# Optimization experiments

Measured on AMD Instinct MI355X. Metric: run time of the kernel, lower is better.

## Reference

```python
import jax, jax.numpy as jnp
import numpy as np

T, TOPK = 512, 2
E, H, D = 8, 2816, 1024


def setup_inputs() -> dict:
    key = jax.random.key(0)
    k1, k2, k3, k4, k5 = jax.random.split(key, 5)
    x = jax.random.normal(k1, (T, D), dtype=jnp.float32)
    expert_indices = jax.random.randint(k2, (T, TOPK), 0, E, dtype=jnp.int64)
    w1 = jax.random.normal(k3, (E, H, D), dtype=jnp.float32)
    w2 = jax.random.normal(k4, (E, H, D), dtype=jnp.float32)
    w3 = jax.random.normal(k5, (E, H, D), dtype=jnp.float32)
    return {"x": x, "expert_indices": expert_indices, "w1": w1, "w2": w2, "w3": w3}


def reference(x, expert_indices, w1, w2, w3):
    # Math identical to: silu(x @ w1[e].T) * (x @ w3[e].T) @ w2[e] for e = expert_indices[t, a].
    # Computed densely over all experts (GEMM-friendly), then gathered per token,
    # which avoids materializing [T, a, H, D] gathered weight tensors.
    h1 = jax.nn.silu(jnp.einsum('ti,ehi->teh', x, w1))   # [T, E, H]
    h3 = jnp.einsum('ti,ehi->teh', x, w3)                # [T, E, H]
    out_all = jnp.einsum('teh,ehi->tei', h1 * h3, w2)    # [T, E, D]
    # gather the top_k selected experts per token -> [T, TOPK, D]
    idx = expert_indices[:, :, None]                     # [T, a, 1]
    expert_outs = jnp.take_along_axis(out_all, idx, axis=1)
    return expert_outs
```

## Files before the change

kernel.cpp:

```cpp
#include <hip/hip_runtime.h>


#define NEXP 8
#define HDIM 2816
#define DDIM 1024
#define NPAIR 1024

typedef unsigned int uint;
typedef unsigned short ushort;
typedef __attribute__((ext_vector_type(8))) short bf16x8;
typedef __attribute__((ext_vector_type(4))) float fvec4;
typedef __attribute__((ext_vector_type(4))) uint uvec4;

__device__ __forceinline__ ushort f2bf(float f) {
    uint u = __builtin_bit_cast(uint, f);
    u += 0x7fff + ((u >> 16) & 1);
    return (ushort)(u >> 16);
}
__device__ __forceinline__ uint pack2(float lo, float hi) {
    return (uint)f2bf(lo) | ((uint)f2bf(hi) << 16);
}
__device__ __forceinline__ uvec4 pack8(fvec4 a, fvec4 b) {
    uvec4 v;
    v.x = pack2(a.x, a.y); v.y = pack2(a.z, a.w);
    v.z = pack2(b.x, b.y); v.w = pack2(b.z, b.w);
    return v;
}

__device__ __forceinline__ void wg_sync_lds() {
    __builtin_amdgcn_sched_barrier(0);
    asm volatile("s_waitcnt lgkmcnt(0)" ::: "memory");
    __builtin_amdgcn_s_barrier();
    __builtin_amdgcn_sched_barrier(0);
}

__global__ __launch_bounds__(1024) void route_kernel(const int* __restrict__ idx,
                                                     int* __restrict__ counts,
                                                     int* __restrict__ lists) {
    int p = threadIdx.x;
    if (p < NEXP) counts[p] = 0;
    __syncthreads();
    int e = idx[p];
    int pos = atomicAdd(&counts[e], 1);
    lists[e * NPAIR + pos] = p;
}

#define LDK 68

#define NCH1 (DDIM / 64)

__global__ __launch_bounds__(512, 4) void h_mfma(const float* __restrict__ x,
                       const float* __restrict__ w1,
                       const float* __restrict__ w3,
                       const int* __restrict__ counts,
                       const int* __restrict__ lists,
                       ushort* __restrict__ hb) {
    const int e = blockIdx.x;
    const int cnt = counts[e];
    const int m0 = blockIdx.z * 128;
    if (m0 >= cnt) return;
    const int h0 = blockIdx.y * 32;

    __shared__ ushort sA[2][128 * LDK];
    __shared__ ushort sB[2][2][32 * LDK];
    __shared__ int sTok[128];
    __shared__ int sPairS[128];

    const int tid = threadIdx.x;
    if (tid < 128) {
        int m = m0 + tid;
        int mc = (m < cnt) ? m : (cnt - 1);
        int p = lists[e * NPAIR + mc];
        sTok[tid] = p >> 1;
        sPairS[tid] = (m < cnt) ? p : -1;
    }
    wg_sync_lds();

    const int arow = tid >> 2;
    const int akg  = (tid & 3) * 16;
    const float* aSrc = x + (size_t)sTok[arow] * DDIM + akg;

    const int bmat = tid >> 8;
    const int brow = (tid >> 3) & 31;
    const int bkg  = (tid & 7) * 8;
    const float* bSrc = (bmat ? w3 : w1) + (size_t)e * HDIM * DDIM
                        + (size_t)(h0 + brow) * DDIM + bkg;

    fvec4 pfA[2][4];
    fvec4 pfB[2][2];

#define P1_ISSUE(S, KC) do { \
    const float* qa = aSrc + (KC) * 64; \
    pfA[S][0] = *(const fvec4*)qa; \
    pfA[S][1] = *(const fvec4*)(qa + 4); \
    pfA[S][2] = *(const fvec4*)(qa + 8); \
    pfA[S][3] = *(const fvec4*)(qa + 12); \
    const float* qb = bSrc + (KC) * 64; \
    pfB[S][0] = *(const fvec4*)qb; \
    pfB[S][1] = *(const fvec4*)(qb + 4); \
} while (0)

#define P1_STAGE(S, B) do { \
    *(uvec4*)&sA[B][arow * LDK + akg] = pack8(pfA[S][0], pfA[S][1]); \
    *(uvec4*)&sA[B][arow * LDK + akg + 8] = pack8(pfA[S][2], pfA[S][3]); \
    *(uvec4*)&sB[B][bmat][brow * LDK + bkg] = pack8(pfB[S][0], pfB[S][1]); \
} while (0)

    const int w = tid >> 6;
    const int wm = w & 3;
    const int wh = w >> 2;
    const int lane = tid & 63;
    const int l16 = lane & 15;
    const int quad = lane >> 4;

    const int ar0 = (wm * 32 + l16) * LDK + quad * 8;
    const int br0 = (wh * 16 + l16) * LDK + quad * 8;

    fvec4 acc[2][2];
    #pragma unroll
    for (int i = 0; i < 2; ++i) { acc[i][0] = (fvec4)0.f; acc[i][1] = (fvec4)0.f; }

    P1_ISSUE(0, 0);
    P1_ISSUE(1, 1);
    P1_STAGE(0, 0);
    wg_sync_lds();

#define P1_BODY(T, CUR) do { \
    bf16x8 a00 = *(const bf16x8*)&sA[CUR][ar0]; \
    bf16x8 a01 = *(const bf16x8*)&sA[CUR][ar0 + 32]; \
    bf16x8 a10 = *(const bf16x8*)&sA[CUR][ar0 + 16 * LDK]; \
    bf16x8 a11 = *(const bf16x8*)&sA[CUR][ar0 + 16 * LDK + 32]; \
    bf16x8 b00 = *(const bf16x8*)&sB[CUR][0][br0]; \
    bf16x8 b01 = *(const bf16x8*)&sB[CUR][0][br0 + 32]; \
    bf16x8 b10 = *(const bf16x8*)&sB[CUR][1][br0]; \
    bf16x8 b11 = *(const bf16x8*)&sB[CUR][1][br0 + 32]; \
    if ((T) + 2 < NCH1) P1_ISSUE(CUR, (T) + 2); \
    acc[0][0] = __builtin_amdgcn_mfma_f32_16x16x32_bf16(a00, b00, acc[0][0], 0, 0, 0); \
    acc[0][1] = __builtin_amdgcn_mfma_f32_16x16x32_bf16(a00, b10, acc[0][1], 0, 0, 0); \
    acc[1][0] = __builtin_amdgcn_mfma_f32_16x16x32_bf16(a10, b00, acc[1][0], 0, 0, 0); \
    acc[1][1] = __builtin_amdgcn_mfma_f32_16x16x32_bf16(a10, b10, acc[1][1], 0, 0, 0); \
    acc[0][0] = __builtin_amdgcn_mfma_f32_16x16x32_bf16(a01, b01, acc[0][0], 0, 0, 0); \
    acc[0][1] = __builtin_amdgcn_mfma_f32_16x16x32_bf16(a01, b11, acc[0][1], 0, 0, 0); \
    acc[1][0] = __builtin_amdgcn_mfma_f32_16x16x32_bf16(a11, b01, acc[1][0], 0, 0, 0); \
    acc[1][1] = __builtin_amdgcn_mfma_f32_16x16x32_bf16(a11, b11, acc[1][1], 0, 0, 0); \
    if ((T) + 1 < NCH1) { \
        P1_STAGE(CUR ^ 1, CUR ^ 1); \
        wg_sync_lds(); \
    } \
} while (0)

    for (int t = 0; t < NCH1; t += 2) {
        P1_BODY(t, 0);
        P1_BODY(t + 1, 1);
    }

    #pragma unroll
    for (int mi = 0; mi < 2; ++mi) {
        #pragma unroll
        for (int r = 0; r < 4; ++r) {
            int mrow = wm * 32 + mi * 16 + quad * 4 + r;
            int p = sPairS[mrow];
            if (p >= 0) {
                float a = acc[mi][0][r];
                float g = acc[mi][1][r];
                float s = a / (1.f + __expf(-a)) * g;
                hb[(size_t)p * HDIM + h0 + wh * 16 + l16] = f2bf(s);
            }
        }
    }
}

#define NCH2 ((HDIM / 4) / 64)

__global__ __launch_bounds__(512, 4) void out_mfma(const float* __restrict__ w2,
                         const int* __restrict__ counts,
                         const int* __restrict__ lists,
                         const ushort* __restrict__ hb,
                         float* __restrict__ out) {
    const int e = blockIdx.x;
    const int cnt = counts[e];
    const int mb = blockIdx.z >> 2;
    const int sk = blockIdx.z & 3;
    const int m0 = mb * 128;
    if (m0 >= cnt) return;
    const int n0 = blockIdx.y * 32;
    const int kbase = sk * (HDIM / 4);

    __shared__ ushort sA[2][128 * LDK];
    __shared__ ushort sB[2][32 * LDK];
    __shared__ int sPairC[128];
    __shared__ int sPairS[128];

    const int tid = threadIdx.x;
    if (tid < 128) {
        int m = m0 + tid;
        int mc = (m < cnt) ? m : (cnt - 1);
        int p = lists[e * NPAIR + mc];
        sPairC[tid] = p;
        sPairS[tid] = (m < cnt) ? p : -1;
    }
    wg_sync_lds();

    const int arow = tid >> 2;
    const int akg  = (tid & 3) * 16;
    const ushort* aSrc = hb + (size_t)sPairC[arow] * HDIM + kbase + akg;

    const int bkp = (tid >> 3) & 31;
    const int bdg = tid & 7;
    const float* bSrc = w2 + (size_t)e * HDIM * DDIM
                        + (size_t)(kbase + 2 * bkp) * DDIM + n0 + bdg * 4;

    uvec4 pfA[2][2];
    fvec4 pfB[2][2];

#define P2_ISSUE(S, KC) do { \
    const ushort* qa = aSrc + (KC) * 64; \
    pfA[S][0] = *(const uvec4*)qa; \
    pfA[S][1] = *(const uvec4*)(qa + 8); \
    if (tid < 256) { \
        const float* qb = bSrc + (size_t)(KC) * 64 * DDIM; \
        pfB[S][0] = *(const fvec4*)qb; \
        pfB[S][1] = *(const fvec4*)(qb + DDIM); \
    } \
} while (0)

#define P2_STAGE(S, B) do { \
    *(uvec4*)&sA[B][arow * LDK + akg] = pfA[S][0]; \
    *(uvec4*)&sA[B][arow * LDK + akg + 8] = pfA[S][1]; \
    if (tid < 256) { \
        _Pragma("unroll") \
        for (int j = 0; j < 4; ++j) \
            *(uint*)&sB[B][(bdg * 4 + j) * LDK + bkp * 2] = pack2(pfB[S][0][j], pfB[S][1][j]); \
    } \
} while (0)

    const int w = tid >> 6;
    const int wm = w & 3;
    const int wh = w >> 2;
    const int lane = tid & 63;
    const int l16 = lane & 15;
    const int quad = lane >> 4;

    const int ar0 = (wm * 32 + l16) * LDK + quad * 8;
    const int br0 = (wh * 16 + l16) * LDK + quad * 8;

    fvec4 acc[2];
    acc[0] = (fvec4)0.f; acc[1] = (fvec4)0.f;

    P2_ISSUE(0, 0);
    P2_ISSUE(1, 1);
    P2_STAGE(0, 0);
    wg_sync_lds();

#define P2_BODY(T, CUR) do { \
    bf16x8 a00 = *(const bf16x8*)&sA[CUR][ar0]; \
    bf16x8 a01 = *(const bf16x8*)&sA[CUR][ar0 + 32]; \
    bf16x8 a10 = *(const bf16x8*)&sA[CUR][ar0 + 16 * LDK]; \
    bf16x8 a11 = *(const bf16x8*)&sA[CUR][ar0 + 16 * LDK + 32]; \
    bf16x8 b0 = *(const bf16x8*)&sB[CUR][br0]; \
    bf16x8 b1 = *(const bf16x8*)&sB[CUR][br0 + 32]; \
    if ((T) + 2 < NCH2) P2_ISSUE(CUR, (T) + 2); \
    acc[0] = __builtin_amdgcn_mfma_f32_16x16x32_bf16(a00, b0, acc[0], 0, 0, 0); \
    acc[1] = __builtin_amdgcn_mfma_f32_16x16x32_bf16(a10, b0, acc[1], 0, 0, 0); \
    acc[0] = __builtin_amdgcn_mfma_f32_16x16x32_bf16(a01, b1, acc[0], 0, 0, 0); \
    acc[1] = __builtin_amdgcn_mfma_f32_16x16x32_bf16(a11, b1, acc[1], 0, 0, 0); \
    if ((T) + 1 < NCH2) { \
        P2_STAGE(CUR ^ 1, CUR ^ 1); \
        wg_sync_lds(); \
    } \
} while (0)

    for (int t = 0; t < NCH2; t += 2) {
        P2_BODY(t, 0);
        if (t + 1 < NCH2) P2_BODY(t + 1, 1);
    }

    #pragma unroll
    for (int mi = 0; mi < 2; ++mi) {
        #pragma unroll
        for (int r = 0; r < 4; ++r) {
            int mrow = wm * 32 + mi * 16 + quad * 4 + r;
            int p = sPairS[mrow];
            if (p >= 0)
                atomicAdd(&out[(size_t)p * DDIM + n0 + wh * 16 + l16], acc[mi][r]);
        }
    }
}

extern "C" void kernel_launch(void* const* d_in, const int* in_sizes, int n_in,
                              void* d_out, int out_size, void* d_ws, size_t ws_size,
                              hipStream_t stream) {
    const float* x   = (const float*)d_in[0];
    const int*   idx = (const int*)d_in[1];
    const float* w1  = (const float*)d_in[2];
    const float* w2  = (const float*)d_in[3];
    const float* w3  = (const float*)d_in[4];
    float* out = (float*)d_out;

    char* ws = (char*)d_ws;
    int*    counts = (int*)ws;
    int*    lists  = (int*)(ws + 1024);
    ushort* hbuf   = (ushort*)(ws + 65536);

    hipMemsetAsync(out, 0, (size_t)out_size * sizeof(float), stream);
    route_kernel<<<1, NPAIR, 0, stream>>>(idx, counts, lists);
    h_mfma<<<dim3(NEXP, HDIM / 32, NPAIR / 128), 512, 0, stream>>>(
        x, w1, w3, counts, lists, hbuf);
    out_mfma<<<dim3(NEXP, DDIM / 32, (NPAIR / 128) * 4), 512, 0, stream>>>(
        w2, counts, lists, hbuf, out);
}
```

Baseline: 345.2 us.

## Load MFMA operands directly from global memory, dropping shared-LDS staging and barriers

Both GEMM kernels stop staging A and B tiles through shared LDS with workgroup barriers. Instead, each wave loads its MFMA fragments straight from global memory into registers, converting them to bf16 in registers. The output kernel uses a small per-wave swizzled LDS buffer to transpose w2. Blocks shrink to 256 threads with a 64-row M tile, and the output kernel's K split goes from 4 to 2. This removes barrier stalls and LDS traffic, but loses data reuse across waves, so the same x and weight rows are fetched by multiple waves through the cache.

```diff
diff --git a/kernel.cpp b/kernel.cpp
--- a/kernel.cpp
+++ b/kernel.cpp
@@ -20,18 +20,11 @@
 __device__ __forceinline__ uint pack2(float lo, float hi) {
     return (uint)f2bf(lo) | ((uint)f2bf(hi) << 16);
 }
-__device__ __forceinline__ uvec4 pack8(fvec4 a, fvec4 b) {
+__device__ __forceinline__ bf16x8 cvt8(fvec4 a, fvec4 b) {
     uvec4 v;
     v.x = pack2(a.x, a.y); v.y = pack2(a.z, a.w);
     v.z = pack2(b.x, b.y); v.w = pack2(b.z, b.w);
-    return v;
-}
-
-__device__ __forceinline__ void wg_sync_lds() {
-    __builtin_amdgcn_sched_barrier(0);
-    asm volatile("s_waitcnt lgkmcnt(0)" ::: "memory");
-    __builtin_amdgcn_s_barrier();
-    __builtin_amdgcn_sched_barrier(0);
+    return __builtin_bit_cast(bf16x8, v);
 }
 
 __global__ __launch_bounds__(1024) void route_kernel(const int* __restrict__ idx,
@@ -45,11 +38,9 @@
     lists[e * NPAIR + pos] = p;
 }
 
-#define LDK 68
-
-#define NCH1 (DDIM / 64)
-
-__global__ __launch_bounds__(512, 4) void h_mfma(const float* __restrict__ x,
+#define NCH1 32
+
+__global__ __launch_bounds__(256, 4) void h_mfma(const float* __restrict__ x,
                        const float* __restrict__ w1,
                        const float* __restrict__ w3,
                        const int* __restrict__ counts,
@@ -57,232 +48,165 @@
                        ushort* __restrict__ hb) {
     const int e = blockIdx.x;
     const int cnt = counts[e];
-    const int m0 = blockIdx.z * 128;
+    const int m0 = blockIdx.z * 64;
     if (m0 >= cnt) return;
     const int h0 = blockIdx.y * 32;
 
-    __shared__ ushort sA[2][128 * LDK];
-    __shared__ ushort sB[2][2][32 * LDK];
-    __shared__ int sTok[128];
-    __shared__ int sPairS[128];
-
     const int tid = threadIdx.x;
-    if (tid < 128) {
-        int m = m0 + tid;
-        int mc = (m < cnt) ? m : (cnt - 1);
-        int p = lists[e * NPAIR + mc];
-        sTok[tid] = p >> 1;
-        sPairS[tid] = (m < cnt) ? p : -1;
-    }
-    wg_sync_lds();
-
-    const int arow = tid >> 2;
-    const int akg  = (tid & 3) * 16;
-    const float* aSrc = x + (size_t)sTok[arow] * DDIM + akg;
-
-    const int bmat = tid >> 8;
-    const int brow = (tid >> 3) & 31;
-    const int bkg  = (tid & 7) * 8;
-    const float* bSrc = (bmat ? w3 : w1) + (size_t)e * HDIM * DDIM
-                        + (size_t)(h0 + brow) * DDIM + bkg;
-
-    fvec4 pfA[2][4];
-    fvec4 pfB[2][2];
-
-#define P1_ISSUE(S, KC) do { \
-    const float* qa = aSrc + (KC) * 64; \
-    pfA[S][0] = *(const fvec4*)qa; \
-    pfA[S][1] = *(const fvec4*)(qa + 4); \
-    pfA[S][2] = *(const fvec4*)(qa + 8); \
-    pfA[S][3] = *(const fvec4*)(qa + 12); \
-    const float* qb = bSrc + (KC) * 64; \
-    pfB[S][0] = *(const fvec4*)qb; \
-    pfB[S][1] = *(const fvec4*)(qb + 4); \
-} while (0)
-
-#define P1_STAGE(S, B) do { \
-    *(uvec4*)&sA[B][arow * LDK + akg] = pack8(pfA[S][0], pfA[S][1]); \
-    *(uvec4*)&sA[B][arow * LDK + akg + 8] = pack8(pfA[S][2], pfA[S][3]); \
-    *(uvec4*)&sB[B][bmat][brow * LDK + bkg] = pack8(pfB[S][0], pfB[S][1]); \
-} while (0)
-
-    const int w = tid >> 6;
-    const int wm = w & 3;
-    const int wh = w >> 2;
+    const int wm = (tid >> 6) & 1;
+    const int wh = tid >> 7;
     const int lane = tid & 63;
     const int l16 = lane & 15;
     const int quad = lane >> 4;
-
-    const int ar0 = (wm * 32 + l16) * LDK + quad * 8;
-    const int br0 = (wh * 16 + l16) * LDK + quad * 8;
+    const int mw = m0 + wm * 32;
+    const int hw = h0 + wh * 16;
+
+    const int* lst = lists + e * NPAIR;
+    int r0 = mw + l16;       int rc0 = (r0 < cnt) ? r0 : (cnt - 1);
+    int r1 = mw + 16 + l16;  int rc1 = (r1 < cnt) ? r1 : (cnt - 1);
+    const float* xa0 = x + (size_t)(lst[rc0] >> 1) * DDIM + quad * 8;
+    const float* xa1 = x + (size_t)(lst[rc1] >> 1) * DDIM + quad * 8;
+    const float* bp1 = w1 + (size_t)e * HDIM * DDIM + (size_t)(hw + l16) * DDIM + quad * 8;
+    const float* bp3 = w3 + (size_t)e * HDIM * DDIM + (size_t)(hw + l16) * DDIM + quad * 8;
+
+    fvec4 pf[2][8];
+
+#define H_ISSUE(S, K) do { \
+    pf[S][0] = *(const fvec4*)(xa0 + (K));     pf[S][1] = *(const fvec4*)(xa0 + (K) + 4); \
+    pf[S][2] = *(const fvec4*)(xa1 + (K));     pf[S][3] = *(const fvec4*)(xa1 + (K) + 4); \
+    pf[S][4] = *(const fvec4*)(bp1 + (K));     pf[S][5] = *(const fvec4*)(bp1 + (K) + 4); \
+    pf[S][6] = *(const fvec4*)(bp3 + (K));     pf[S][7] = *(const fvec4*)(bp3 + (K) + 4); \
+} while (0)
 
     fvec4 acc[2][2];
     #pragma unroll
     for (int i = 0; i < 2; ++i) { acc[i][0] = (fvec4)0.f; acc[i][1] = (fvec4)0.f; }
 
-    P1_ISSUE(0, 0);
-    P1_ISSUE(1, 1);
-    P1_STAGE(0, 0);
-    wg_sync_lds();
-
-#define P1_BODY(T, CUR) do { \
-    bf16x8 a00 = *(const bf16x8*)&sA[CUR][ar0]; \
-    bf16x8 a01 = *(const bf16x8*)&sA[CUR][ar0 + 32]; \
-    bf16x8 a10 = *(const bf16x8*)&sA[CUR][ar0 + 16 * LDK]; \
-    bf16x8 a11 = *(const bf16x8*)&sA[CUR][ar0 + 16 * LDK + 32]; \
-    bf16x8 b00 = *(const bf16x8*)&sB[CUR][0][br0]; \
-    bf16x8 b01 = *(const bf16x8*)&sB[CUR][0][br0 + 32]; \
-    bf16x8 b10 = *(const bf16x8*)&sB[CUR][1][br0]; \
-    bf16x8 b11 = *(const bf16x8*)&sB[CUR][1][br0 + 32]; \
-    if ((T) + 2 < NCH1) P1_ISSUE(CUR, (T) + 2); \
-    acc[0][0] = __builtin_amdgcn_mfma_f32_16x16x32_bf16(a00, b00, acc[0][0], 0, 0, 0); \
-    acc[0][1] = __builtin_amdgcn_mfma_f32_16x16x32_bf16(a00, b10, acc[0][1], 0, 0, 0); \
-    acc[1][0] = __builtin_amdgcn_mfma_f32_16x16x32_bf16(a10, b00, acc[1][0], 0, 0, 0); \
-    acc[1][1] = __builtin_amdgcn_mfma_f32_16x16x32_bf16(a10, b10, acc[1][1], 0, 0, 0); \
-    acc[0][0] = __builtin_amdgcn_mfma_f32_16x16x32_bf16(a01, b01, acc[0][0], 0, 0, 0); \
-    acc[0][1] = __builtin_amdgcn_mfma_f32_16x16x32_bf16(a01, b11, acc[0][1], 0, 0, 0); \
-    acc[1][0] = __builtin_amdgcn_mfma_f32_16x16x32_bf16(a11, b01, acc[1][0], 0, 0, 0); \
-    acc[1][1] = __builtin_amdgcn_mfma_f32_16x16x32_bf16(a11, b11, acc[1][1], 0, 0, 0); \
-    if ((T) + 1 < NCH1) { \
-        P1_STAGE(CUR ^ 1, CUR ^ 1); \
-        wg_sync_lds(); \
-    } \
+    H_ISSUE(0, 0);
+    H_ISSUE(1, 32);
+
+#define H_BODY(T, S) do { \
+    bf16x8 a0 = cvt8(pf[S][0], pf[S][1]); \
+    bf16x8 a1 = cvt8(pf[S][2], pf[S][3]); \
+    bf16x8 b1 = cvt8(pf[S][4], pf[S][5]); \
+    bf16x8 b3 = cvt8(pf[S][6], pf[S][7]); \
+    if ((T) + 2 < NCH1) H_ISSUE(S, ((T) + 2) * 32); \
+    acc[0][0] = __builtin_amdgcn_mfma_f32_16x16x32_bf16(a0, b1, acc[0][0], 0, 0, 0); \
+    acc[0][1] = __builtin_amdgcn_mfma_f32_16x16x32_bf16(a0, b3, acc[0][1], 0, 0, 0); \
+    acc[1][0] = __builtin_amdgcn_mfma_f32_16x16x32_bf16(a1, b1, acc[1][0], 0, 0, 0); \
+    acc[1][1] = __builtin_amdgcn_mfma_f32_16x16x32_bf16(a1, b3, acc[1][1], 0, 0, 0); \
 } while (0)
 
     for (int t = 0; t < NCH1; t += 2) {
-        P1_BODY(t, 0);
-        P1_BODY(t + 1, 1);
+        H_BODY(t, 0);
+        H_BODY(t + 1, 1);
     }
 
     #pragma unroll
     for (int mi = 0; mi < 2; ++mi) {
         #pragma unroll
         for (int r = 0; r < 4; ++r) {
-            int mrow = wm * 32 + mi * 16 + quad * 4 + r;
-            int p = sPairS[mrow];
-            if (p >= 0) {
+            int row = mw + mi * 16 + quad * 4 + r;
+            if (row < cnt) {
+                int p = lst[row];
                 float a = acc[mi][0][r];
                 float g = acc[mi][1][r];
                 float s = a / (1.f + __expf(-a)) * g;
-                hb[(size_t)p * HDIM + h0 + wh * 16 + l16] = f2bf(s);
+                hb[(size_t)p * HDIM + hw + l16] = f2bf(s);
             }
         }
     }
 }
 
-#define NCH2 ((HDIM / 4) / 64)
-
-__global__ __launch_bounds__(512, 4) void out_mfma(const float* __restrict__ w2,
+#define NCH2 ((HDIM / 2) / 64)
+
+__global__ __launch_bounds__(256, 4) void out_mfma(const float* __restrict__ w2,
                          const int* __restrict__ counts,
                          const int* __restrict__ lists,
                          const ushort* __restrict__ hb,
                          float* __restrict__ out) {
     const int e = blockIdx.x;
     const int cnt = counts[e];
-    const int mb = blockIdx.z >> 2;
-    const int sk = blockIdx.z & 3;
-    const int m0 = mb * 128;
+    const int mb = blockIdx.z >> 1;
+    const int sk = blockIdx.z & 1;
+    const int m0 = mb * 64;
     if (m0 >= cnt) return;
     const int n0 = blockIdx.y * 32;
-    const int kbase = sk * (HDIM / 4);
-
-    __shared__ ushort sA[2][128 * LDK];
-    __shared__ ushort sB[2][32 * LDK];
-    __shared__ int sPairC[128];
-    __shared__ int sPairS[128];
+    const int kbase = sk * (HDIM / 2);
+
+    __shared__ ushort sB[4][16 * 64];
 
     const int tid = threadIdx.x;
-    if (tid < 128) {
-        int m = m0 + tid;
-        int mc = (m < cnt) ? m : (cnt - 1);
-        int p = lists[e * NPAIR + mc];
-        sPairC[tid] = p;
-        sPairS[tid] = (m < cnt) ? p : -1;
-    }
-    wg_sync_lds();
-
-    const int arow = tid >> 2;
-    const int akg  = (tid & 3) * 16;
-    const ushort* aSrc = hb + (size_t)sPairC[arow] * HDIM + kbase + akg;
-
-    const int bkp = (tid >> 3) & 31;
-    const int bdg = tid & 7;
-    const float* bSrc = w2 + (size_t)e * HDIM * DDIM
-                        + (size_t)(kbase + 2 * bkp) * DDIM + n0 + bdg * 4;
-
-    uvec4 pfA[2][2];
-    fvec4 pfB[2][2];
-
-#define P2_ISSUE(S, KC) do { \
-    const ushort* qa = aSrc + (KC) * 64; \
-    pfA[S][0] = *(const uvec4*)qa; \
-    pfA[S][1] = *(const uvec4*)(qa + 8); \
-    if (tid < 256) { \
-        const float* qb = bSrc + (size_t)(KC) * 64 * DDIM; \
-        pfB[S][0] = *(const fvec4*)qb; \
-        pfB[S][1] = *(const fvec4*)(qb + DDIM); \
-    } \
-} while (0)
-
-#define P2_STAGE(S, B) do { \
-    *(uvec4*)&sA[B][arow * LDK + akg] = pfA[S][0]; \
-    *(uvec4*)&sA[B][arow * LDK + akg + 8] = pfA[S][1]; \
-    if (tid < 256) { \
-        _Pragma("unroll") \
-        for (int j = 0; j < 4; ++j) \
-            *(uint*)&sB[B][(bdg * 4 + j) * LDK + bkp * 2] = pack2(pfB[S][0][j], pfB[S][1][j]); \
-    } \
-} while (0)
-
-    const int w = tid >> 6;
-    const int wm = w & 3;
-    const int wh = w >> 2;
+    const int wid = tid >> 6;
+    const int wm = wid & 1;
+    const int wd = wid >> 1;
     const int lane = tid & 63;
     const int l16 = lane & 15;
     const int quad = lane >> 4;
-
-    const int ar0 = (wm * 32 + l16) * LDK + quad * 8;
-    const int br0 = (wh * 16 + l16) * LDK + quad * 8;
+    const int lg = lane >> 3;
+    const int lo = lane & 7;
+    const int mw = m0 + wm * 32;
+    const int dw = n0 + wd * 16;
+
+    const int* lst = lists + e * NPAIR;
+    int r0 = mw + l16;       int rc0 = (r0 < cnt) ? r0 : (cnt - 1);
+    int r1 = mw + 16 + l16;  int rc1 = (r1 < cnt) ? r1 : (cnt - 1);
+    const ushort* ha0 = hb + (size_t)lst[rc0] * HDIM + kbase + quad * 8;
+    const ushort* ha1 = hb + (size_t)lst[rc1] * HDIM + kbase + quad * 8;
+    const float* bp = w2 + (size_t)e * HDIM * DDIM + (size_t)(kbase + lane) * DDIM + dw;
+
+    uvec4 pa[2][4];
+    fvec4 pb[2][4];
+
+#define O_ISSUE(S, C) do { \
+    const ushort* qa0 = ha0 + (C) * 64; \
+    const ushort* qa1 = ha1 + (C) * 64; \
+    pa[S][0] = *(const uvec4*)qa0;        pa[S][1] = *(const uvec4*)(qa0 + 32); \
+    pa[S][2] = *(const uvec4*)qa1;        pa[S][3] = *(const uvec4*)(qa1 + 32); \
+    const float* qb = bp + (size_t)(C) * 64 * DDIM; \
+    pb[S][0] = *(const fvec4*)qb;         pb[S][1] = *(const fvec4*)(qb + 4); \
+    pb[S][2] = *(const fvec4*)(qb + 8);   pb[S][3] = *(const fvec4*)(qb + 12); \
+} while (0)
+
+    ushort* myB = &sB[wid][0];
 
     fvec4 acc[2];
     acc[0] = (fvec4)0.f; acc[1] = (fvec4)0.f;
 
-    P2_ISSUE(0, 0);
-    P2_ISSUE(1, 1);
-    P2_STAGE(0, 0);
-    wg_sync_lds();
-
-#define P2_BODY(T, CUR) do { \
-    bf16x8 a00 = *(const bf16x8*)&sA[CUR][ar0]; \
-    bf16x8 a01 = *(const bf16x8*)&sA[CUR][ar0 + 32]; \
-    bf16x8 a10 = *(const bf16x8*)&sA[CUR][ar0 + 16 * LDK]; \
-    bf16x8 a11 = *(const bf16x8*)&sA[CUR][ar0 + 16 * LDK + 32]; \
-    bf16x8 b0 = *(const bf16x8*)&sB[CUR][br0]; \
-    bf16x8 b1 = *(const bf16x8*)&sB[CUR][br0 + 32]; \
-    if ((T) + 2 < NCH2) P2_ISSUE(CUR, (T) + 2); \
+    O_ISSUE(0, 0);
+    O_ISSUE(1, 1);
+
+#define O_BODY(T, S) do { \
+    _Pragma("unroll") \
+    for (int j = 0; j < 16; ++j) \
+        myB[j * 64 + (((lg ^ j) & 7) << 3) + lo] = f2bf(pb[S][j >> 2][j & 3]); \
+    bf16x8 a00 = __builtin_bit_cast(bf16x8, pa[S][0]); \
+    bf16x8 a01 = __builtin_bit_cast(bf16x8, pa[S][1]); \
+    bf16x8 a10 = __builtin_bit_cast(bf16x8, pa[S][2]); \
+    bf16x8 a11 = __builtin_bit_cast(bf16x8, pa[S][3]); \
+    if ((T) + 2 < NCH2) O_ISSUE(S, (T) + 2); \
+    bf16x8 b0 = *(const bf16x8*)&myB[l16 * 64 + ((((0 + quad) ^ l16) & 7) << 3)]; \
+    bf16x8 b1 = *(const bf16x8*)&myB[l16 * 64 + ((((4 + quad) ^ l16) & 7) << 3)]; \
     acc[0] = __builtin_amdgcn_mfma_f32_16x16x32_bf16(a00, b0, acc[0], 0, 0, 0); \
     acc[1] = __builtin_amdgcn_mfma_f32_16x16x32_bf16(a10, b0, acc[1], 0, 0, 0); \
     acc[0] = __builtin_amdgcn_mfma_f32_16x16x32_bf16(a01, b1, acc[0], 0, 0, 0); \
     acc[1] = __builtin_amdgcn_mfma_f32_16x16x32_bf16(a11, b1, acc[1], 0, 0, 0); \
-    if ((T) + 1 < NCH2) { \
-        P2_STAGE(CUR ^ 1, CUR ^ 1); \
-        wg_sync_lds(); \
-    } \
 } while (0)
 
     for (int t = 0; t < NCH2; t += 2) {
-        P2_BODY(t, 0);
-        if (t + 1 < NCH2) P2_BODY(t + 1, 1);
+        O_BODY(t, 0);
+        O_BODY(t + 1, 1);
     }
 
     #pragma unroll
     for (int mi = 0; mi < 2; ++mi) {
         #pragma unroll
         for (int r = 0; r < 4; ++r) {
-            int mrow = wm * 32 + mi * 16 + quad * 4 + r;
-            int p = sPairS[mrow];
-            if (p >= 0)
-                atomicAdd(&out[(size_t)p * DDIM + n0 + wh * 16 + l16], acc[mi][r]);
+            int row = mw + mi * 16 + quad * 4 + r;
+            if (row < cnt) {
+                int p = lst[row];
+                atomicAdd(&out[(size_t)p * DDIM + dw + l16], acc[mi][r]);
+            }
         }
     }
 }
@@ -304,8 +228,8 @@
 
     hipMemsetAsync(out, 0, (size_t)out_size * sizeof(float), stream);
     route_kernel<<<1, NPAIR, 0, stream>>>(idx, counts, lists);
-    h_mfma<<<dim3(NEXP, HDIM / 32, NPAIR / 128), 512, 0, stream>>>(
+    h_mfma<<<dim3(NEXP, HDIM / 32, NPAIR / 64), 256, 0, stream>>>(
         x, w1, w3, counts, lists, hbuf);
-    out_mfma<<<dim3(NEXP, DDIM / 32, (NPAIR / 128) * 4), 512, 0, stream>>>(
+    out_mfma<<<dim3(NEXP, DDIM / 32, (NPAIR / 64) * 2), 256, 0, stream>>>(
         w2, counts, lists, hbuf, out);
 }
```

Result: slower. 596.2 us (+72.7%).

## Drop LDS staging in h_mfma and load MFMA fragments directly from global memory

Applied to the files above, without the earlier changes.

The gate/up projection kernel now reads each wave's x and w1/w3 fragments straight from global memory into registers. It converts them to bf16 in registers and feeds the MFMAs, with a two-stage software prefetch and no shared memory or barriers. The tile shrinks to 64 rows per 256-thread block, and the grid doubles along z. This removes LDS writes, LDS reads and workgroup synchronisation. The cost is lost on-chip reuse: weight and activation data are fetched redundantly across waves and blocks, which leans on L2 and uses a less coalesced per-lane access pattern.

```diff
diff --git a/kernel.cpp b/kernel.cpp
--- a/kernel.cpp
+++ b/kernel.cpp
@@ -25,6 +25,9 @@
     v.x = pack2(a.x, a.y); v.y = pack2(a.z, a.w);
     v.z = pack2(b.x, b.y); v.w = pack2(b.z, b.w);
     return v;
+}
+__device__ __forceinline__ bf16x8 cvt8(fvec4 a, fvec4 b) {
+    return __builtin_bit_cast(bf16x8, pack8(a, b));
 }
 
 __device__ __forceinline__ void wg_sync_lds() {
@@ -45,11 +48,9 @@
     lists[e * NPAIR + pos] = p;
 }
 
-#define LDK 68
-
-#define NCH1 (DDIM / 64)
-
-__global__ __launch_bounds__(512, 4) void h_mfma(const float* __restrict__ x,
+#define NCH1 32
+
+__global__ __launch_bounds__(256, 2) void h_mfma(const float* __restrict__ x,
                        const float* __restrict__ w1,
                        const float* __restrict__ w3,
                        const int* __restrict__ counts,
@@ -57,119 +58,115 @@
                        ushort* __restrict__ hb) {
     const int e = blockIdx.x;
     const int cnt = counts[e];
-    const int m0 = blockIdx.z * 128;
+    const int m0 = blockIdx.z * 64;
     if (m0 >= cnt) return;
     const int h0 = blockIdx.y * 32;
 
-    __shared__ ushort sA[2][128 * LDK];
-    __shared__ ushort sB[2][2][32 * LDK];
-    __shared__ int sTok[128];
-    __shared__ int sPairS[128];
-
     const int tid = threadIdx.x;
-    if (tid < 128) {
-        int m = m0 + tid;
-        int mc = (m < cnt) ? m : (cnt - 1);
-        int p = lists[e * NPAIR + mc];
-        sTok[tid] = p >> 1;
-        sPairS[tid] = (m < cnt) ? p : -1;
-    }
-    wg_sync_lds();
-
-    const int arow = tid >> 2;
-    const int akg  = (tid & 3) * 16;
-    const float* aSrc = x + (size_t)sTok[arow] * DDIM + akg;
-
-    const int bmat = tid >> 8;
-    const int brow = (tid >> 3) & 31;
-    const int bkg  = (tid & 7) * 8;
-    const float* bSrc = (bmat ? w3 : w1) + (size_t)e * HDIM * DDIM
-                        + (size_t)(h0 + brow) * DDIM + bkg;
-
-    fvec4 pfA[2][4];
-    fvec4 pfB[2][2];
-
-#define P1_ISSUE(S, KC) do { \
-    const float* qa = aSrc + (KC) * 64; \
-    pfA[S][0] = *(const fvec4*)qa; \
-    pfA[S][1] = *(const fvec4*)(qa + 4); \
-    pfA[S][2] = *(const fvec4*)(qa + 8); \
-    pfA[S][3] = *(const fvec4*)(qa + 12); \
-    const float* qb = bSrc + (KC) * 64; \
-    pfB[S][0] = *(const fvec4*)qb; \
-    pfB[S][1] = *(const fvec4*)(qb + 4); \
-} while (0)
-
-#define P1_STAGE(S, B) do { \
-    *(uvec4*)&sA[B][arow * LDK + akg] = pack8(pfA[S][0], pfA[S][1]); \
-    *(uvec4*)&sA[B][arow * LDK + akg + 8] = pack8(pfA[S][2], pfA[S][3]); \
-    *(uvec4*)&sB[B][bmat][brow * LDK + bkg] = pack8(pfB[S][0], pfB[S][1]); \
-} while (0)
-
-    const int w = tid >> 6;
-    const int wm = w & 3;
-    const int wh = w >> 2;
+    const int wm = (tid >> 6) & 1;
+    const int wh = tid >> 7;
     const int lane = tid & 63;
     const int l16 = lane & 15;
     const int quad = lane >> 4;
-
-    const int ar0 = (wm * 32 + l16) * LDK + quad * 8;
-    const int br0 = (wh * 16 + l16) * LDK + quad * 8;
-
-    fvec4 acc[2][2];
-    #pragma unroll
-    for (int i = 0; i < 2; ++i) { acc[i][0] = (fvec4)0.f; acc[i][1] = (fvec4)0.f; }
-
-    P1_ISSUE(0, 0);
-    P1_ISSUE(1, 1);
-    P1_STAGE(0, 0);
-    wg_sync_lds();
-
-#define P1_BODY(T, CUR) do { \
-    bf16x8 a00 = *(const bf16x8*)&sA[CUR][ar0]; \
-    bf16x8 a01 = *(const bf16x8*)&sA[CUR][ar0 + 32]; \
-    bf16x8 a10 = *(const bf16x8*)&sA[CUR][ar0 + 16 * LDK]; \
-    bf16x8 a11 = *(const bf16x8*)&sA[CUR][ar0 + 16 * LDK + 32]; \
-    bf16x8 b00 = *(const bf16x8*)&sB[CUR][0][br0]; \
-    bf16x8 b01 = *(const bf16x8*)&sB[CUR][0][br0 + 32]; \
-    bf16x8 b10 = *(const bf16x8*)&sB[CUR][1][br0]; \
-    bf16x8 b11 = *(const bf16x8*)&sB[CUR][1][br0 + 32]; \
-    if ((T) + 2 < NCH1) P1_ISSUE(CUR, (T) + 2); \
-    acc[0][0] = __builtin_amdgcn_mfma_f32_16x16x32_bf16(a00, b00, acc[0][0], 0, 0, 0); \
-    acc[0][1] = __builtin_amdgcn_mfma_f32_16x16x32_bf16(a00, b10, acc[0][1], 0, 0, 0); \
-    acc[1][0] = __builtin_amdgcn_mfma_f32_16x16x32_bf16(a10, b00, acc[1][0], 0, 0, 0); \
-    acc[1][1] = __builtin_amdgcn_mfma_f32_16x16x32_bf16(a10, b10, acc[1][1], 0, 0, 0); \
-    acc[0][0] = __builtin_amdgcn_mfma_f32_16x16x32_bf16(a01, b01, acc[0][0], 0, 0, 0); \
-    acc[0][1] = __builtin_amdgcn_mfma_f32_16x16x32_bf16(a01, b11, acc[0][1], 0, 0, 0); \
-    acc[1][0] = __builtin_amdgcn_mfma_f32_16x16x32_bf16(a11, b01, acc[1][0], 0, 0, 0); \
-    acc[1][1] = __builtin_amdgcn_mfma_f32_16x16x32_bf16(a11, b11, acc[1][1], 0, 0, 0); \
-    if ((T) + 1 < NCH1) { \
-        P1_STAGE(CUR ^ 1, CUR ^ 1); \
-        wg_sync_lds(); \
-    } \
-} while (0)
-
-    for (int t = 0; t < NCH1; t += 2) {
-        P1_BODY(t, 0);
-        P1_BODY(t + 1, 1);
-    }
-
+    const int mw = m0 + wm * 32;
+    const int hw = h0 + wh * 16;
+
+    const int* lst = lists + e * NPAIR;
+    int r0 = mw + l16;       int rc0 = (r0 < cnt) ? r0 : (cnt - 1);
+    int r1 = mw + 16 + l16;  int rc1 = (r1 < cnt) ? r1 : (cnt - 1);
+    const float* xa0 = x + (size_t)(lst[rc0] >> 1) * DDIM + quad * 8;
+    const float* xa1 = x + (size_t)(lst[rc1] >> 1) * DDIM + quad * 8;
+    const float* bp1 = w1 + (size_t)e * HDIM * DDIM + (size_t)(hw + l16) * DDIM + quad * 8;
+    const float* bp3 = w3 + (size_t)e * HDIM * DDIM + (size_t)(hw + l16) * DDIM + quad * 8;
+
+    fvec4 a0lo0, a0hi0, a1lo0, a1hi0, b1lo0, b1hi0, b3lo0, b3hi0;
+    fvec4 a0lo1, a0hi1, a1lo1, a1hi1, b1lo1, b1hi1, b3lo1, b3hi1;
+
+#define H_ISSUE(S, KO) do { \
+    a0lo##S = *(const fvec4*)(xa0 + (KO)); a0hi##S = *(const fvec4*)(xa0 + (KO) + 4); \
+    a1lo##S = *(const fvec4*)(xa1 + (KO)); a1hi##S = *(const fvec4*)(xa1 + (KO) + 4); \
+    b1lo##S = *(const fvec4*)(bp1 + (KO)); b1hi##S = *(const fvec4*)(bp1 + (KO) + 4); \
+    b3lo##S = *(const fvec4*)(bp3 + (KO)); b3hi##S = *(const fvec4*)(bp3 + (KO) + 4); \
+} while (0)
+
+    fvec4 acc00 = (fvec4)0.f, acc01 = (fvec4)0.f;
+    fvec4 acc10 = (fvec4)0.f, acc11 = (fvec4)0.f;
+
+#define H_MFMA(S) do { \
+    bf16x8 fa0 = cvt8(a0lo##S, a0hi##S); \
+    bf16x8 fa1 = cvt8(a1lo##S, a1hi##S); \
+    bf16x8 fb1 = cvt8(b1lo##S, b1hi##S); \
+    bf16x8 fb3 = cvt8(b3lo##S, b3hi##S); \
+    acc00 = __builtin_amdgcn_mfma_f32_16x16x32_bf16(fa0, fb1, acc00, 0, 0, 0); \
+    acc01 = __builtin_amdgcn_mfma_f32_16x16x32_bf16(fa0, fb3, acc01, 0, 0, 0); \
+    acc10 = __builtin_amdgcn_mfma_f32_16x16x32_bf16(fa1, fb1, acc10, 0, 0, 0); \
+    acc11 = __builtin_amdgcn_mfma_f32_16x16x32_bf16(fa1, fb3, acc11, 0, 0, 0); \
+} while (0)
+
+    H_ISSUE(0, 0);
+    H_ISSUE(1, 32);
+
+    int t = 0;
+    for (; t < NCH1 - 4; t += 2) {
+        {
+            bf16x8 fa0 = cvt8(a0lo0, a0hi0), fa1 = cvt8(a1lo0, a1hi0);
+            bf16x8 fb1 = cvt8(b1lo0, b1hi0), fb3 = cvt8(b3lo0, b3hi0);
+            H_ISSUE(0, (t + 2) * 32);
+            acc00 = __builtin_amdgcn_mfma_f32_16x16x32_bf16(fa0, fb1, acc00, 0, 0, 0);
+            acc01 = __builtin_amdgcn_mfma_f32_16x16x32_bf16(fa0, fb3, acc01, 0, 0, 0);
+            acc10 = __builtin_amdgcn_mfma_f32_16x16x32_bf16(fa1, fb1, acc10, 0, 0, 0);
+            acc11 = __builtin_amdgcn_mfma_f32_16x16x32_bf16(fa1, fb3, acc11, 0, 0, 0);
+        }
+        {
+            bf16x8 fa0 = cvt8(a0lo1, a0hi1), fa1 = cvt8(a1lo1, a1hi1);
+            bf16x8 fb1 = cvt8(b1lo1, b1hi1), fb3 = cvt8(b3lo1, b3hi1);
+            H_ISSUE(1, (t + 3) * 32);
+            acc00 = __builtin_amdgcn_mfma_f32_16x16x32_bf16(fa0, fb1, acc00, 0, 0, 0);
+            acc01 = __builtin_amdgcn_mfma_f32_16x16x32_bf16(fa0, fb3, acc01, 0, 0, 0);
+            acc10 = __builtin_amdgcn_mfma_f32_16x16x32_bf16(fa1, fb1, acc10, 0, 0, 0);
+            acc11 = __builtin_amdgcn_mfma_f32_16x16x32_bf16(fa1, fb3, acc11, 0, 0, 0);
+        }
+    }
+    {
+        bf16x8 fa0 = cvt8(a0lo0, a0hi0), fa1 = cvt8(a1lo0, a1hi0);
+        bf16x8 fb1 = cvt8(b1lo0, b1hi0), fb3 = cvt8(b3lo0, b3hi0);
+        H_ISSUE(0, (NCH1 - 2) * 32);
+        acc00 = __builtin_amdgcn_mfma_f32_16x16x32_bf16(fa0, fb1, acc00, 0, 0, 0);
+        acc01 = __builtin_amdgcn_mfma_f32_16x16x32_bf16(fa0, fb3, acc01, 0, 0, 0);
+        acc10 = __builtin_amdgcn_mfma_f32_16x16x32_bf16(fa1, fb1, acc10, 0, 0, 0);
+        acc11 = __builtin_amdgcn_mfma_f32_16x16x32_bf16(fa1, fb3, acc11, 0, 0, 0);
+    }
+    {
+        bf16x8 fa0 = cvt8(a0lo1, a0hi1), fa1 = cvt8(a1lo1, a1hi1);
+        bf16x8 fb1 = cvt8(b1lo1, b1hi1), fb3 = cvt8(b3lo1, b3hi1);
+        H_ISSUE(1, (NCH1 - 1) * 32);
+        acc00 = __builtin_amdgcn_mfma_f32_16x16x32_bf16(fa0, fb1, acc00, 0, 0, 0);
+        acc01 = __builtin_amdgcn_mfma_f32_16x16x32_bf16(fa0, fb3, acc01, 0, 0, 0);
+        acc10 = __builtin_amdgcn_mfma_f32_16x16x32_bf16(fa1, fb1, acc10, 0, 0, 0);
+        acc11 = __builtin_amdgcn_mfma_f32_16x16x32_bf16(fa1, fb3, acc11, 0, 0, 0);
+    }
+    H_MFMA(0);
+    H_MFMA(1);
+
+    fvec4 accA[2][2];
+    accA[0][0] = acc00; accA[0][1] = acc01; accA[1][0] = acc10; accA[1][1] = acc11;
     #pragma unroll
     for (int mi = 0; mi < 2; ++mi) {
         #pragma unroll
         for (int r = 0; r < 4; ++r) {
-            int mrow = wm * 32 + mi * 16 + quad * 4 + r;
-            int p = sPairS[mrow];
-            if (p >= 0) {
-                float a = acc[mi][0][r];
-                float g = acc[mi][1][r];
+            int row = mw + mi * 16 + quad * 4 + r;
+            if (row < cnt) {
+                int p = lst[row];
+                float a = accA[mi][0][r];
+                float g = accA[mi][1][r];
                 float s = a / (1.f + __expf(-a)) * g;
-                hb[(size_t)p * HDIM + h0 + wh * 16 + l16] = f2bf(s);
+                hb[(size_t)p * HDIM + hw + l16] = f2bf(s);
             }
         }
     }
 }
 
+#define LDK 68
 #define NCH2 ((HDIM / 4) / 64)
 
 __global__ __launch_bounds__(512, 4) void out_mfma(const float* __restrict__ w2,
@@ -304,7 +301,7 @@
 
     hipMemsetAsync(out, 0, (size_t)out_size * sizeof(float), stream);
     route_kernel<<<1, NPAIR, 0, stream>>>(idx, counts, lists);
-    h_mfma<<<dim3(NEXP, HDIM / 32, NPAIR / 128), 512, 0, stream>>>(
+    h_mfma<<<dim3(NEXP, HDIM / 32, NPAIR / 64), 256, 0, stream>>>(
         x, w1, w3, counts, lists, hbuf);
     out_mfma<<<dim3(NEXP, DDIM / 32, (NPAIR / 128) * 4), 512, 0, stream>>>(
         w2, counts, lists, hbuf, out);
```

Result: slower. 465.1 us (+34.7%).

## Stream A fragments from registers and stage wide-K weight chunks in h_mfma

Applied to the files above, without the earlier changes.

Rewrites the first-stage expert GEMM so each wave loads its own token rows of x straight from global memory into registers and converts them to bf16 fragments, with no shared-memory staging for A. The w1/w3 tiles are staged in 256-wide K chunks, giving four double-buffered chunks instead of sixteen 64-wide ones, so there are fewer workgroup barriers. Each wave now owns 16 rows and computes all 32 hidden columns for both gate and up. The cost is more global loads and repeated bf16 conversion of x per block, and a larger LDS footprint for B.

```diff
diff --git a/kernel.cpp b/kernel.cpp
--- a/kernel.cpp
+++ b/kernel.cpp
@@ -11,6 +11,7 @@
 typedef __attribute__((ext_vector_type(8))) short bf16x8;
 typedef __attribute__((ext_vector_type(4))) float fvec4;
 typedef __attribute__((ext_vector_type(4))) uint uvec4;
+typedef __attribute__((ext_vector_type(2))) uint uvec2;
 
 __device__ __forceinline__ ushort f2bf(float f) {
     uint u = __builtin_bit_cast(uint, f);
@@ -25,6 +26,9 @@
     v.x = pack2(a.x, a.y); v.y = pack2(a.z, a.w);
     v.z = pack2(b.x, b.y); v.w = pack2(b.z, b.w);
     return v;
+}
+__device__ __forceinline__ bf16x8 cvt8(fvec4 a, fvec4 b) {
+    return __builtin_bit_cast(bf16x8, pack8(a, b));
 }
 
 __device__ __forceinline__ void wg_sync_lds() {
@@ -45,9 +49,7 @@
     lists[e * NPAIR + pos] = p;
 }
 
-#define LDK 68
-
-#define NCH1 (DDIM / 64)
+#define LDB1 264
 
 __global__ __launch_bounds__(512, 4) void h_mfma(const float* __restrict__ x,
                        const float* __restrict__ w1,
@@ -61,115 +63,113 @@
     if (m0 >= cnt) return;
     const int h0 = blockIdx.y * 32;
 
-    __shared__ ushort sA[2][128 * LDK];
-    __shared__ ushort sB[2][2][32 * LDK];
-    __shared__ int sTok[128];
-    __shared__ int sPairS[128];
+    __shared__ ushort sB[2][2][32 * LDB1];
 
     const int tid = threadIdx.x;
-    if (tid < 128) {
-        int m = m0 + tid;
-        int mc = (m < cnt) ? m : (cnt - 1);
-        int p = lists[e * NPAIR + mc];
-        sTok[tid] = p >> 1;
-        sPairS[tid] = (m < cnt) ? p : -1;
-    }
-    wg_sync_lds();
-
-    const int arow = tid >> 2;
-    const int akg  = (tid & 3) * 16;
-    const float* aSrc = x + (size_t)sTok[arow] * DDIM + akg;
-
-    const int bmat = tid >> 8;
-    const int brow = (tid >> 3) & 31;
-    const int bkg  = (tid & 7) * 8;
-    const float* bSrc = (bmat ? w3 : w1) + (size_t)e * HDIM * DDIM
-                        + (size_t)(h0 + brow) * DDIM + bkg;
-
-    fvec4 pfA[2][4];
-    fvec4 pfB[2][2];
-
-#define P1_ISSUE(S, KC) do { \
-    const float* qa = aSrc + (KC) * 64; \
-    pfA[S][0] = *(const fvec4*)qa; \
-    pfA[S][1] = *(const fvec4*)(qa + 4); \
-    pfA[S][2] = *(const fvec4*)(qa + 8); \
-    pfA[S][3] = *(const fvec4*)(qa + 12); \
-    const float* qb = bSrc + (KC) * 64; \
-    pfB[S][0] = *(const fvec4*)qb; \
-    pfB[S][1] = *(const fvec4*)(qb + 4); \
-} while (0)
-
-#define P1_STAGE(S, B) do { \
-    *(uvec4*)&sA[B][arow * LDK + akg] = pack8(pfA[S][0], pfA[S][1]); \
-    *(uvec4*)&sA[B][arow * LDK + akg + 8] = pack8(pfA[S][2], pfA[S][3]); \
-    *(uvec4*)&sB[B][bmat][brow * LDK + bkg] = pack8(pfB[S][0], pfB[S][1]); \
-} while (0)
-
     const int w = tid >> 6;
-    const int wm = w & 3;
-    const int wh = w >> 2;
     const int lane = tid & 63;
     const int l16 = lane & 15;
     const int quad = lane >> 4;
 
-    const int ar0 = (wm * 32 + l16) * LDK + quad * 8;
-    const int br0 = (wh * 16 + l16) * LDK + quad * 8;
-
-    fvec4 acc[2][2];
+    const int* lst = lists + e * NPAIR;
+    int arow = m0 + w * 16 + l16;
+    int arc = (arow < cnt) ? arow : (cnt - 1);
+    const float* xa = x + (size_t)(lst[arc] >> 1) * DDIM + quad * 8;
+
+    const float* stB1 = w1 + (size_t)e * HDIM * DDIM + (size_t)(h0 + w) * DDIM + lane * 4;
+    const float* stB3 = w3 + (size_t)e * HDIM * DDIM + (size_t)(h0 + w) * DDIM + lane * 4;
+
+    fvec4 pb0, pb1, pb2, pb3, pb4, pb5, pb6, pb7;
+    fvec4 pa0x, pa0y, pa1x, pa1y, pa2x, pa2y, pa3x, pa3y;
+    fvec4 acc00 = (fvec4)0.f, acc01 = (fvec4)0.f;
+    fvec4 acc10 = (fvec4)0.f, acc11 = (fvec4)0.f;
+
+#define P1_ISSUE_B(KC) do { \
+    pb0 = *(const fvec4*)(stB1 + (KC) * 256 + 0 * 8 * DDIM); \
+    pb1 = *(const fvec4*)(stB1 + (KC) * 256 + 1 * 8 * DDIM); \
+    pb2 = *(const fvec4*)(stB1 + (KC) * 256 + 2 * 8 * DDIM); \
+    pb3 = *(const fvec4*)(stB1 + (KC) * 256 + 3 * 8 * DDIM); \
+    pb4 = *(const fvec4*)(stB3 + (KC) * 256 + 0 * 8 * DDIM); \
+    pb5 = *(const fvec4*)(stB3 + (KC) * 256 + 1 * 8 * DDIM); \
+    pb6 = *(const fvec4*)(stB3 + (KC) * 256 + 2 * 8 * DDIM); \
+    pb7 = *(const fvec4*)(stB3 + (KC) * 256 + 3 * 8 * DDIM); \
+} while (0)
+
+#define P1_WRITE_B(BUF) do { \
+    *(uvec2*)&sB[BUF][0][(w +  0) * LDB1 + lane * 4] = (uvec2){pack2(pb0.x, pb0.y), pack2(pb0.z, pb0.w)}; \
+    *(uvec2*)&sB[BUF][0][(w +  8) * LDB1 + lane * 4] = (uvec2){pack2(pb1.x, pb1.y), pack2(pb1.z, pb1.w)}; \
+    *(uvec2*)&sB[BUF][0][(w + 16) * LDB1 + lane * 4] = (uvec2){pack2(pb2.x, pb2.y), pack2(pb2.z, pb2.w)}; \
+    *(uvec2*)&sB[BUF][0][(w + 24) * LDB1 + lane * 4] = (uvec2){pack2(pb3.x, pb3.y), pack2(pb3.z, pb3.w)}; \
+    *(uvec2*)&sB[BUF][1][(w +  0) * LDB1 + lane * 4] = (uvec2){pack2(pb4.x, pb4.y), pack2(pb4.z, pb4.w)}; \
+    *(uvec2*)&sB[BUF][1][(w +  8) * LDB1 + lane * 4] = (uvec2){pack2(pb5.x, pb5.y), pack2(pb5.z, pb5.w)}; \
+    *(uvec2*)&sB[BUF][1][(w + 16) * LDB1 + lane * 4] = (uvec2){pack2(pb6.x, pb6.y), pack2(pb6.z, pb6.w)}; \
+    *(uvec2*)&sB[BUF][1][(w + 24) * LDB1 + lane * 4] = (uvec2){pack2(pb7.x, pb7.y), pack2(pb7.z, pb7.w)}; \
+} while (0)
+
+#define BFRAG(BUF, MAT, HF, KS) \
+    (*(const bf16x8*)&sB[BUF][MAT][((HF) * 16 + l16) * LDB1 + (KS) * 32 + quad * 8])
+
+#define P1_KSTEP(BUF, KS, SL, RELK) do { \
+    bf16x8 af = cvt8(pa##SL##x, pa##SL##y); \
+    bf16x8 b00 = BFRAG(BUF, 0, 0, KS); \
+    bf16x8 b01 = BFRAG(BUF, 0, 1, KS); \
+    bf16x8 b10 = BFRAG(BUF, 1, 0, KS); \
+    bf16x8 b11 = BFRAG(BUF, 1, 1, KS); \
+    if ((RELK) < 32) { \
+        pa##SL##x = *(const fvec4*)(xa + (RELK) * 32); \
+        pa##SL##y = *(const fvec4*)(xa + (RELK) * 32 + 4); \
+    } \
+    acc00 = __builtin_amdgcn_mfma_f32_16x16x32_bf16(af, b00, acc00, 0, 0, 0); \
+    acc01 = __builtin_amdgcn_mfma_f32_16x16x32_bf16(af, b01, acc01, 0, 0, 0); \
+    acc10 = __builtin_amdgcn_mfma_f32_16x16x32_bf16(af, b10, acc10, 0, 0, 0); \
+    acc11 = __builtin_amdgcn_mfma_f32_16x16x32_bf16(af, b11, acc11, 0, 0, 0); \
+} while (0)
+
+#define P1_CHUNK(T, BUF) do { \
+    P1_KSTEP(BUF, 0, 0, (T) * 8 + 4); \
+    P1_KSTEP(BUF, 1, 1, (T) * 8 + 5); \
+    P1_KSTEP(BUF, 2, 2, (T) * 8 + 6); \
+    P1_KSTEP(BUF, 3, 3, (T) * 8 + 7); \
+    P1_KSTEP(BUF, 4, 0, (T) * 8 + 8); \
+    P1_KSTEP(BUF, 5, 1, (T) * 8 + 9); \
+    P1_KSTEP(BUF, 6, 2, (T) * 8 + 10); \
+    P1_KSTEP(BUF, 7, 3, (T) * 8 + 11); \
+} while (0)
+
+    P1_ISSUE_B(0);
+    pa0x = *(const fvec4*)(xa +  0); pa0y = *(const fvec4*)(xa +  4);
+    pa1x = *(const fvec4*)(xa + 32); pa1y = *(const fvec4*)(xa + 36);
+    pa2x = *(const fvec4*)(xa + 64); pa2y = *(const fvec4*)(xa + 68);
+    pa3x = *(const fvec4*)(xa + 96); pa3y = *(const fvec4*)(xa + 100);
+    P1_WRITE_B(0);
+    P1_ISSUE_B(1);
+    wg_sync_lds();
+
+    P1_CHUNK(0, 0);
+    P1_WRITE_B(1); P1_ISSUE_B(2); wg_sync_lds();
+    P1_CHUNK(1, 1);
+    P1_WRITE_B(0); P1_ISSUE_B(3); wg_sync_lds();
+    P1_CHUNK(2, 0);
+    P1_WRITE_B(1);                 wg_sync_lds();
+    P1_CHUNK(3, 1);
+
     #pragma unroll
-    for (int i = 0; i < 2; ++i) { acc[i][0] = (fvec4)0.f; acc[i][1] = (fvec4)0.f; }
-
-    P1_ISSUE(0, 0);
-    P1_ISSUE(1, 1);
-    P1_STAGE(0, 0);
-    wg_sync_lds();
-
-#define P1_BODY(T, CUR) do { \
-    bf16x8 a00 = *(const bf16x8*)&sA[CUR][ar0]; \
-    bf16x8 a01 = *(const bf16x8*)&sA[CUR][ar0 + 32]; \
-    bf16x8 a10 = *(const bf16x8*)&sA[CUR][ar0 + 16 * LDK]; \
-    bf16x8 a11 = *(const bf16x8*)&sA[CUR][ar0 + 16 * LDK + 32]; \
-    bf16x8 b00 = *(const bf16x8*)&sB[CUR][0][br0]; \
-    bf16x8 b01 = *(const bf16x8*)&sB[CUR][0][br0 + 32]; \
-    bf16x8 b10 = *(const bf16x8*)&sB[CUR][1][br0]; \
-    bf16x8 b11 = *(const bf16x8*)&sB[CUR][1][br0 + 32]; \
-    if ((T) + 2 < NCH1) P1_ISSUE(CUR, (T) + 2); \
-    acc[0][0] = __builtin_amdgcn_mfma_f32_16x16x32_bf16(a00, b00, acc[0][0], 0, 0, 0); \
-    acc[0][1] = __builtin_amdgcn_mfma_f32_16x16x32_bf16(a00, b10, acc[0][1], 0, 0, 0); \
-    acc[1][0] = __builtin_amdgcn_mfma_f32_16x16x32_bf16(a10, b00, acc[1][0], 0, 0, 0); \
-    acc[1][1] = __builtin_amdgcn_mfma_f32_16x16x32_bf16(a10, b10, acc[1][1], 0, 0, 0); \
-    acc[0][0] = __builtin_amdgcn_mfma_f32_16x16x32_bf16(a01, b01, acc[0][0], 0, 0, 0); \
-    acc[0][1] = __builtin_amdgcn_mfma_f32_16x16x32_bf16(a01, b11, acc[0][1], 0, 0, 0); \
-    acc[1][0] = __builtin_amdgcn_mfma_f32_16x16x32_bf16(a11, b01, acc[1][0], 0, 0, 0); \
-    acc[1][1] = __builtin_amdgcn_mfma_f32_16x16x32_bf16(a11, b11, acc[1][1], 0, 0, 0); \
-    if ((T) + 1 < NCH1) { \
-        P1_STAGE(CUR ^ 1, CUR ^ 1); \
-        wg_sync_lds(); \
-    } \
-} while (0)
-
-    for (int t = 0; t < NCH1; t += 2) {
-        P1_BODY(t, 0);
-        P1_BODY(t + 1, 1);
-    }
-
-    #pragma unroll
-    for (int mi = 0; mi < 2; ++mi) {
+    for (int hf = 0; hf < 2; ++hf) {
         #pragma unroll
         for (int r = 0; r < 4; ++r) {
-            int mrow = wm * 32 + mi * 16 + quad * 4 + r;
-            int p = sPairS[mrow];
-            if (p >= 0) {
-                float a = acc[mi][0][r];
-                float g = acc[mi][1][r];
+            int row = m0 + w * 16 + quad * 4 + r;
+            if (row < cnt) {
+                int p = lst[row];
+                float a = (hf == 0) ? acc00[r] : acc01[r];
+                float g = (hf == 0) ? acc10[r] : acc11[r];
                 float s = a / (1.f + __expf(-a)) * g;
-                hb[(size_t)p * HDIM + h0 + wh * 16 + l16] = f2bf(s);
+                hb[(size_t)p * HDIM + h0 + hf * 16 + l16] = f2bf(s);
             }
         }
     }
 }
 
+#define LDK 68
 #define NCH2 ((HDIM / 4) / 64)
 
 __global__ __launch_bounds__(512, 4) void out_mfma(const float* __restrict__ w2,
```

New measurement: 334.2 us. -3.2%, faster.
